# Optimization experiments

Hardware: AMD Instinct MI355X
Metric: run time of the kernel (lower is better)

The kernel has to match this reference:

```python
import jax, jax.numpy as jnp
import numpy as np

NUM_NETS = 100_000
PINS_PER_NET = 5
NUM_PINS = NUM_NETS * PINS_PER_NET
XL, XH, YL, YH = 0.0, 1000.0, 0.0, 1000.0
NUM_BINS_X = 512
NUM_BINS_Y = 512
BIN_SIZE_X = (XH - XL) / NUM_BINS_X
BIN_SIZE_Y = (YH - YL) / NUM_BINS_Y
NUM_H_TRACKS = 100.0
NUM_V_TRACKS = 100.0
MAX_RATE = 2.0
MIN_RATE = 1.0 / MAX_RATE


def setup_inputs() -> dict:
    key = jax.random.key(0)
    k1, k2, k3 = jax.random.split(key, 3)
    px = jax.random.uniform(k1, (NUM_PINS,), jnp.float32, XL, XH)
    py = jax.random.uniform(k2, (NUM_PINS,), jnp.float32, YL, YH)
    pin_pos = jnp.concatenate([px, py])  # [2*num_pins]: x then y
    netpin_start = (jnp.arange(NUM_NETS + 1, dtype=jnp.int32) * PINS_PER_NET)
    flat_netpin = jax.random.permutation(k3, NUM_PINS).astype(jnp.int32)
    net_weights = jnp.ones((NUM_NETS,), jnp.float32)
    return {"pin_pos": pin_pos, "netpin_start": netpin_start,
            "flat_netpin": flat_netpin, "net_weights": net_weights}


def reference(pin_pos, netpin_start, flat_netpin, net_weights):
    num_pins = flat_netpin.shape[0]
    # segment id of each flat pin slot (which net it belongs to)
    seg = jnp.searchsorted(netpin_start, jnp.arange(num_pins, dtype=netpin_start.dtype), side="right") - 1
    x = pin_pos[flat_netpin]                     # [num_pins]
    y = pin_pos[num_pins + flat_netpin]          # [num_pins]
    # per-net bounding boxes
    x_min = jax.ops.segment_min(x, seg, num_segments=NUM_NETS)
    x_max = jax.ops.segment_max(x, seg, num_segments=NUM_NETS)
    y_min = jax.ops.segment_min(y, seg, num_segments=NUM_NETS)
    y_max = jax.ops.segment_max(y, seg, num_segments=NUM_NETS)
    # fractional overlap of each net bbox with each bin column/row
    ex = XL + BIN_SIZE_X * jnp.arange(NUM_BINS_X + 1, dtype=pin_pos.dtype)
    ey = YL + BIN_SIZE_Y * jnp.arange(NUM_BINS_Y + 1, dtype=pin_pos.dtype)
    ox = jnp.maximum(jnp.minimum(x_max[:, None], ex[None, 1:]) -
                     jnp.maximum(x_min[:, None], ex[None, :-1]), 0.0)  # [N, Bx]
    oy = jnp.maximum(jnp.minimum(y_max[:, None], ey[None, 1:]) -
                     jnp.maximum(y_min[:, None], ey[None, :-1]), 0.0)  # [N, By]
    # RUDY: horizontal density wt/(y_max-y_min), vertical density wt/(x_max-x_min)
    wh = net_weights / (y_max - y_min)
    wv = net_weights / (x_max - x_min)
    h_map = jnp.einsum("nx,ny->xy", ox * wh[:, None], oy)
    v_map = jnp.einsum("nx,ny->xy", ox * wv[:, None], oy)
    h_map = h_map * (1.0 / (BIN_SIZE_X * NUM_H_TRACKS))
    v_map = v_map * (1.0 / (BIN_SIZE_Y * NUM_V_TRACKS))
    route = jnp.maximum(jnp.abs(h_map), jnp.abs(v_map))
    return jnp.clip(route * route, MIN_RATE, MAX_RATE)
```

## Files before the change

kernel.cpp:

```cpp
#include <hip/hip_runtime.h>

#define NUM_NETS     100000
#define PINS_PER_NET 5
#define NUM_PINS     (NUM_NETS * PINS_PER_NET)
#define NB           512
#define BIN_H        1.953125f
#define INV_H        0.512f
#define OUT_SCALE    (1.0f / 195.3125f)

#define SW           8
#define NSTRIPES     (NB / SW)
#define CAP          24576

#define FXS          2097152.0f
#define INV_FXS      (1.0f / 2097152.0f)

__global__ void zero_kernel(int* __restrict__ gcur) {
    gcur[threadIdx.x] = 0;
}

__global__ __launch_bounds__(256) void bbox_emit_kernel(
        const float* __restrict__ pin_pos,
        const int*   __restrict__ flat_netpin,
        const float* __restrict__ net_weights,
        int* __restrict__ gcur,
        float4* __restrict__ bucket) {
    __shared__ int lcnt[NSTRIPES];
    __shared__ int lbase[NSTRIPES];
    int tid = threadIdx.x;
    if (tid < NSTRIPES) lcnt[tid] = 0;
    __syncthreads();

    int n = blockIdx.x * 256 + tid;
    bool valid = n < NUM_NETS;
    float xmn = 1e30f, xmx = -1e30f, ymn = 1e30f, ymx = -1e30f;
    float wh = 0.f, wv = 0.f;
    int kx1 = 0, kx2 = 0;
    if (valid) {
#pragma unroll
        for (int p = 0; p < PINS_PER_NET; ++p) {
            int pi  = flat_netpin[n * PINS_PER_NET + p];
            float x = pin_pos[pi];
            float y = pin_pos[NUM_PINS + pi];
            xmn = fminf(xmn, x); xmx = fmaxf(xmx, x);
            ymn = fminf(ymn, y); ymx = fmaxf(ymx, y);
        }
        float w = net_weights[n];
        wh = w / (ymx - ymn);
        wv = w / (xmx - xmn);
        kx1 = min(NB - 1, (int)(xmn * INV_H));
        kx2 = min(NB - 1, (int)(xmx * INV_H));
#pragma unroll
        for (int cx = 0; cx < 2; ++cx) {
            int kx = cx ? kx2 : kx1;
            int s0 = kx >> 3;
            atomicAdd(&lcnt[s0], 2);
            if (kx + 1 < NB && ((kx + 1) >> 3) != s0)
                atomicAdd(&lcnt[(kx + 1) >> 3], 2);
        }
    }
    __syncthreads();
    if (tid < NSTRIPES) {
        lbase[tid] = atomicAdd(&gcur[tid], lcnt[tid]);
        lcnt[tid] = 0;
    }
    __syncthreads();
    if (valid) {
#pragma unroll
        for (int cx = 0; cx < 2; ++cx) {
            int   kx = cx ? kx2 : kx1;
            float xc = cx ? xmx : xmn;
            int s0 = kx >> 3;
            int s1 = (kx + 1 < NB) ? ((kx + 1) >> 3) : s0;
#pragma unroll
            for (int cy = 0; cy < 2; ++cy) {
                float yc = cy ? ymx : ymn;
                float sg = ((cx ^ cy) ? -1.0f : 1.0f);
                float4 item = make_float4(xc, yc, sg * wh, sg * wv);
                {
                    int rank = atomicAdd(&lcnt[s0], 1);
                    int pos  = lbase[s0] + rank;
                    if (pos < CAP) bucket[(size_t)s0 * CAP + pos] = item;
                }
                if (s1 != s0) {
                    int rank = atomicAdd(&lcnt[s1], 1);
                    int pos  = lbase[s1] + rank;
                    if (pos < CAP) bucket[(size_t)s1 * CAP + pos] = item;
                }
            }
        }
    }
}

__global__ __launch_bounds__(1024) void stripe_finish_kernel(
        const float4* __restrict__ bucket,
        const int* __restrict__ gcur,
        float* __restrict__ Th,  float* __restrict__ Tv,
        int* __restrict__ flag,
        float* __restrict__ out) {
    __shared__ int   acc[2 * SW * NB];
    __shared__ float wsc[32];
    __shared__ float offHs[2][NB];
    __shared__ float offVs[2][NB];
    int st  = blockIdx.x;
    int tid = threadIdx.x;
    int x0  = st * SW;
    int* accH = acc;
    int* accV = acc + SW * NB;
    float* fH = (float*)accH;
    float* fV = (float*)accV;

    for (int k = tid; k < 2 * SW * NB; k += 1024) acc[k] = 0;
    __syncthreads();

    int cnt = min(gcur[st], CAP);
    const float4* bk = bucket + (size_t)st * CAP;
    for (int q = tid; q < cnt; q += 1024) {
        float4 it = bk[q];
        int kx = min(NB - 1, (int)(it.x * INV_H));
        int ky = min(NB - 1, (int)(it.y * INV_H));
        float dx0 = (kx + 1) * BIN_H - it.x;
        float dx1 = it.x - kx * BIN_H;
        float dy0 = (ky + 1) * BIN_H - it.y;
        float dy1 = it.y - ky * BIN_H;
        bool y1ok = (ky + 1) < NB;
        int c = kx - x0;
#pragma unroll
        for (int cc = 0; cc < 2; ++cc) {
            int col = c + cc;
            if ((unsigned)col < SW) {
                float dx = cc ? dx1 : dx0;
                int b = col * NB + ky;
                atomicAdd(&accH[b], __float2int_rn(it.z * dx * dy0 * FXS));
                atomicAdd(&accV[b], __float2int_rn(it.w * dx * dy0 * FXS));
                if (y1ok) {
                    atomicAdd(&accH[b + 1], __float2int_rn(it.z * dx * dy1 * FXS));
                    atomicAdd(&accV[b + 1], __float2int_rn(it.w * dx * dy1 * FXS));
                }
            }
        }
    }
    __syncthreads();

    int half = tid >> 9;
    int y    = tid & 511;
    int lane = tid & 63;
    int wv16 = tid >> 6;
    int wrow0 = half * 8;
#pragma unroll
    for (int rp = 0; rp < 4; ++rp) {
        int row = rp * 2 + half;
        float vH = (float)accH[row * NB + y] * INV_FXS;
        float vV = (float)accV[row * NB + y] * INV_FXS;
#pragma unroll
        for (int o = 1; o < 64; o <<= 1) {
            float a = __shfl_up(vH, o);
            float b = __shfl_up(vV, o);
            if (lane >= o) { vH += a; vV += b; }
        }
        if (lane == 63) { wsc[wv16] = vH; wsc[16 + wv16] = vV; }
        __syncthreads();
        float oh = 0.f, ov = 0.f;
        for (int j = wrow0; j < wv16; ++j) { oh += wsc[j]; ov += wsc[16 + j]; }
        fH[row * NB + y] = vH + oh;
        fV[row * NB + y] = vV + ov;
        __syncthreads();
    }

    if (tid < NB) {
        float f = 0.f;
#pragma unroll
        for (int rr = 0; rr < SW; ++rr) {
            int i = rr * NB + tid;
            f += fH[i]; fH[i] = f;
        }
        __hip_atomic_store(&Th[st * NB + tid], f, __ATOMIC_RELAXED,
                           __HIP_MEMORY_SCOPE_AGENT);
    } else {
        int yy = tid - NB;
        float f = 0.f;
#pragma unroll
        for (int rr = 0; rr < SW; ++rr) {
            int i = rr * NB + yy;
            f += fV[i]; fV[i] = f;
        }
        __hip_atomic_store(&Tv[st * NB + yy], f, __ATOMIC_RELAXED,
                           __HIP_MEMORY_SCOPE_AGENT);
    }
    __syncthreads();
    if (tid == 0) {
        __threadfence();
        __hip_atomic_store(&flag[st], 1, __ATOMIC_RELEASE,
                           __HIP_MEMORY_SCOPE_AGENT);
    }

    if (tid < st) {
        while (__hip_atomic_load(&flag[tid], __ATOMIC_ACQUIRE,
                                 __HIP_MEMORY_SCOPE_AGENT) == 0) { }
    }
    __syncthreads();
    {
        float sh = 0.f, sv = 0.f;
        for (int s2 = half; s2 < st; s2 += 2) {
            sh += __hip_atomic_load(&Th[s2 * NB + y], __ATOMIC_RELAXED,
                                    __HIP_MEMORY_SCOPE_AGENT);
            sv += __hip_atomic_load(&Tv[s2 * NB + y], __ATOMIC_RELAXED,
                                    __HIP_MEMORY_SCOPE_AGENT);
        }
        offHs[half][y] = sh;
        offVs[half][y] = sv;
    }
    __syncthreads();

    {
        float offh = offHs[0][y] + offHs[1][y];
        float offv = offVs[0][y] + offVs[1][y];
#pragma unroll
        for (int r2 = 0; r2 < 4; ++r2) {
            int rr = half * 4 + r2;
            float h = fabsf(fH[rr * NB + y] + offh) * OUT_SCALE;
            float v = fabsf(fV[rr * NB + y] + offv) * OUT_SCALE;
            float m = fmaxf(h, v);
            out[(x0 + rr) * NB + y] = fminf(fmaxf(m * m, 0.5f), 2.0f);
        }
    }
}

__global__ void scatter_kernel(const float* __restrict__ pin_pos,
                               const int*   __restrict__ flat_netpin,
                               const float* __restrict__ net_weights,
                               float* __restrict__ Uh,
                               float* __restrict__ Uv) {
    int n = blockIdx.x * blockDim.x + threadIdx.x;
    if (n >= NUM_NETS) return;
    float xmn = 1e30f, xmx = -1e30f, ymn = 1e30f, ymx = -1e30f;
#pragma unroll
    for (int p = 0; p < PINS_PER_NET; ++p) {
        int pi  = flat_netpin[n * PINS_PER_NET + p];
        float x = pin_pos[pi];
        float y = pin_pos[NUM_PINS + pi];
        xmn = fminf(xmn, x); xmx = fmaxf(xmx, x);
        ymn = fminf(ymn, y); ymx = fmaxf(ymx, y);
    }
    float w  = net_weights[n];
    float wh = w / (ymx - ymn), wv = w / (xmx - xmn);
    int kx1 = min(NB - 1, (int)(xmn * INV_H));
    int kx2 = min(NB - 1, (int)(xmx * INV_H));
    int ky1 = min(NB - 1, (int)(ymn * INV_H));
    int ky2 = min(NB - 1, (int)(ymx * INV_H));
    int   xi[4] = { kx1, kx1 + 1, kx2, kx2 + 1 };
    float xv[4] = { (kx1 + 1) * BIN_H - xmn,  xmn - kx1 * BIN_H,
                    xmx - (kx2 + 1) * BIN_H,  kx2 * BIN_H - xmx };
    int   yi[4] = { ky1, ky1 + 1, ky2, ky2 + 1 };
    float yv[4] = { (ky1 + 1) * BIN_H - ymn,  ymn - ky1 * BIN_H,
                    ymx - (ky2 + 1) * BIN_H,  ky2 * BIN_H - ymx };
#pragma unroll
    for (int a = 0; a < 4; ++a) {
        if (xi[a] >= NB) continue;
#pragma unroll
        for (int b2 = 0; b2 < 4; ++b2) {
            if (yi[b2] >= NB) continue;
            float prod = xv[a] * yv[b2];
            atomicAdd(&Uh[xi[a] * NB + yi[b2]], wh * prod);
            atomicAdd(&Uv[xi[a] * NB + yi[b2]], wv * prod);
        }
    }
}

__global__ void fb_rowscan_kernel(float* __restrict__ Uh, float* __restrict__ Uv) {
    __shared__ float sh[NB];
    __shared__ float sv[NB];
    int rr = blockIdx.x, t = threadIdx.x;
    sh[t] = Uh[rr * NB + t];
    sv[t] = Uv[rr * NB + t];
    __syncthreads();
#pragma unroll
    for (int off = 1; off < NB; off <<= 1) {
        float a = (t >= off) ? sh[t - off] : 0.0f;
        float b = (t >= off) ? sv[t - off] : 0.0f;
        __syncthreads();
        sh[t] += a; sv[t] += b;
        __syncthreads();
    }
    Uh[rr * NB + t] = sh[t];
    Uv[rr * NB + t] = sv[t];
}

__global__ void fb_colscan_kernel(const float* __restrict__ Uh,
                                  const float* __restrict__ Uv,
                                  float* __restrict__ out) {
    int t = blockIdx.x * blockDim.x + threadIdx.x;
    if (t >= NB) return;
    float sh = 0.f, sv = 0.f;
    for (int i = 0; i < NB; ++i) {
        sh += Uh[i * NB + t];
        sv += Uv[i * NB + t];
        float h = fabsf(sh) * OUT_SCALE;
        float v = fabsf(sv) * OUT_SCALE;
        float m = fmaxf(h, v);
        out[i * NB + t] = fminf(fmaxf(m * m, 0.5f), 2.0f);
    }
}

extern "C" void kernel_launch(void* const* d_in, const int* in_sizes, int n_in,
                              void* d_out, int out_size, void* d_ws, size_t ws_size,
                              hipStream_t stream) {
    const float* pin_pos     = (const float*)d_in[0];
    const int*   flat_netpin = (const int*)d_in[2];
    const float* net_weights = (const float*)d_in[3];
    float* out = (float*)d_out;
    float* ws  = (float*)d_ws;

    const size_t o_cur = 0;
    const size_t o_flg = 64;
    const size_t o_bkt = 128;
    const size_t o_Th  = o_bkt + (size_t)NSTRIPES * CAP * 4;
    const size_t o_Tv  = o_Th + (size_t)NSTRIPES * NB;
    const size_t need  = o_Tv + (size_t)NSTRIPES * NB;

    if (ws_size < need * sizeof(float)) {
        float* Uh = ws;
        float* Uv = ws + (size_t)NB * NB;
        hipMemsetAsync(ws, 0, 2 * (size_t)NB * NB * sizeof(float), stream);
        scatter_kernel<<<(NUM_NETS + 255) / 256, 256, 0, stream>>>(
            pin_pos, flat_netpin, net_weights, Uh, Uv);
        fb_rowscan_kernel<<<NB, NB, 0, stream>>>(Uh, Uv);
        fb_colscan_kernel<<<2, 256, 0, stream>>>(Uh, Uv, out);
        return;
    }

    int*    gcur   = (int*)(ws + o_cur);
    int*    flg    = (int*)(ws + o_flg);
    float4* bucket = (float4*)(ws + o_bkt);
    float*  Th     = ws + o_Th;
    float*  Tv     = ws + o_Tv;

    zero_kernel<<<1, 128, 0, stream>>>(gcur);

    bbox_emit_kernel<<<(NUM_NETS + 255) / 256, 256, 0, stream>>>(
        pin_pos, flat_netpin, net_weights, gcur, bucket);

    stripe_finish_kernel<<<NSTRIPES, 1024, 0, stream>>>(
        bucket, gcur, Th, Tv, flg, out);
}
```

Baseline: 50.56 us.

## Batch bucket emission in pairs, enlarge emit blocks, vectorize zeroing, sleep in spin

The emit kernel now reserves two bucket slots per x-corner with one shared atomic and writes the ymin/ymax items back to back, halving local atomics and making stores contiguous. Emit blocks grow from 256 to 1024 threads, giving fewer global atomics on the stripe counters, and empty stripes skip their global atomic. The stripe kernel zeroes shared memory with int4 stores, and the cross-block flag spin loop adds s_sleep to cut memory polling pressure. Larger blocks mean more contention on the LDS counters and fewer blocks to spread across CUs.

```diff
diff --git a/kernel.cpp b/kernel.cpp
--- a/kernel.cpp
+++ b/kernel.cpp
@@ -15,11 +15,11 @@
 #define FXS          2097152.0f
 #define INV_FXS      (1.0f / 2097152.0f)
 
-__global__ void zero_kernel(int* __restrict__ gcur) {
-    gcur[threadIdx.x] = 0;
-}
-
-__global__ __launch_bounds__(256) void bbox_emit_kernel(
+__global__ void zero_kernel(int* __restrict__ p) {
+    if (threadIdx.x < 128) p[threadIdx.x] = 0;
+}
+
+__global__ __launch_bounds__(1024) void bbox_emit_kernel(
         const float* __restrict__ pin_pos,
         const int*   __restrict__ flat_netpin,
         const float* __restrict__ net_weights,
@@ -31,7 +31,7 @@
     if (tid < NSTRIPES) lcnt[tid] = 0;
     __syncthreads();
 
-    int n = blockIdx.x * 256 + tid;
+    int n = blockIdx.x * 1024 + tid;
     bool valid = n < NUM_NETS;
     float xmn = 1e30f, xmx = -1e30f, ymn = 1e30f, ymx = -1e30f;
     float wh = 0.f, wv = 0.f;
@@ -61,7 +61,8 @@
     }
     __syncthreads();
     if (tid < NSTRIPES) {
-        lbase[tid] = atomicAdd(&gcur[tid], lcnt[tid]);
+        int c = lcnt[tid];
+        lbase[tid] = c ? atomicAdd(&gcur[tid], c) : 0;
         lcnt[tid] = 0;
     }
     __syncthreads();
@@ -71,21 +72,26 @@
             int   kx = cx ? kx2 : kx1;
             float xc = cx ? xmx : xmn;
             int s0 = kx >> 3;
-            int s1 = (kx + 1 < NB) ? ((kx + 1) >> 3) : s0;
-#pragma unroll
-            for (int cy = 0; cy < 2; ++cy) {
-                float yc = cy ? ymx : ymn;
-                float sg = ((cx ^ cy) ? -1.0f : 1.0f);
-                float4 item = make_float4(xc, yc, sg * wh, sg * wv);
-                {
-                    int rank = atomicAdd(&lcnt[s0], 1);
-                    int pos  = lbase[s0] + rank;
-                    if (pos < CAP) bucket[(size_t)s0 * CAP + pos] = item;
+            int s1 = (kx + 1 < NB && ((kx + 1) >> 3) != s0) ? ((kx + 1) >> 3) : -1;
+            float sg0 = cx ? -1.0f : 1.0f;
+            float4 item0 = make_float4(xc, ymn,  sg0 * wh,  sg0 * wv);
+            float4 item1 = make_float4(xc, ymx, -sg0 * wh, -sg0 * wv);
+            {
+                int rank = atomicAdd(&lcnt[s0], 2);
+                int pos  = lbase[s0] + rank;
+                if (pos + 1 < CAP) {
+                    float4* dst = &bucket[(size_t)s0 * CAP + pos];
+                    dst[0] = item0;
+                    dst[1] = item1;
                 }
-                if (s1 != s0) {
-                    int rank = atomicAdd(&lcnt[s1], 1);
-                    int pos  = lbase[s1] + rank;
-                    if (pos < CAP) bucket[(size_t)s1 * CAP + pos] = item;
+            }
+            if (s1 >= 0) {
+                int rank = atomicAdd(&lcnt[s1], 2);
+                int pos  = lbase[s1] + rank;
+                if (pos + 1 < CAP) {
+                    float4* dst = &bucket[(size_t)s1 * CAP + pos];
+                    dst[0] = item0;
+                    dst[1] = item1;
                 }
             }
         }
@@ -110,7 +116,11 @@
     float* fH = (float*)accH;
     float* fV = (float*)accV;
 
-    for (int k = tid; k < 2 * SW * NB; k += 1024) acc[k] = 0;
+    {
+        int4* a4 = (int4*)&acc[tid * 8];
+        a4[0] = make_int4(0, 0, 0, 0);
+        a4[1] = make_int4(0, 0, 0, 0);
+    }
     __syncthreads();
 
     int cnt = min(gcur[st], CAP);
@@ -196,7 +206,9 @@
 
     if (tid < st) {
         while (__hip_atomic_load(&flag[tid], __ATOMIC_ACQUIRE,
-                                 __HIP_MEMORY_SCOPE_AGENT) == 0) { }
+                                 __HIP_MEMORY_SCOPE_AGENT) == 0) {
+            __builtin_amdgcn_s_sleep(2);
+        }
     }
     __syncthreads();
     {
@@ -335,9 +347,9 @@
     float*  Th     = ws + o_Th;
     float*  Tv     = ws + o_Tv;
 
-    zero_kernel<<<1, 128, 0, stream>>>(gcur);
-
-    bbox_emit_kernel<<<(NUM_NETS + 255) / 256, 256, 0, stream>>>(
+    zero_kernel<<<1, 128, 0, stream>>>((int*)ws);
+
+    bbox_emit_kernel<<<(NUM_NETS + 1023) / 1024, 1024, 0, stream>>>(
         pin_pos, flat_netpin, net_weights, gcur, bucket);
 
     stripe_finish_kernel<<<NSTRIPES, 1024, 0, stream>>>(
```

Measured after the change: 54.20 us. 1.07x slower.
